# Performance work log

Measured on AMD Instinct MI355X. Metric: run time of the kernel, lower is better.

## Reference

```python
import jax, jax.numpy as jnp
import numpy as np

B, T, C, HS = 8, 4096, 1024, 64  # batch, seq, n_embd, head_size


def setup_inputs() -> dict:
    key = jax.random.key(0)
    kx, kk, kq, kv = jax.random.split(key, 4)
    x = jax.random.normal(kx, (B, T, C), dtype=jnp.float32)
    # bias-free linear weights, stored as [in, out] like flax kernels
    s = 1.0 / np.sqrt(C)
    Wk = jax.random.normal(kk, (C, HS), dtype=jnp.float32) * s
    Wq = jax.random.normal(kq, (C, HS), dtype=jnp.float32) * s
    Wv = jax.random.normal(kv, (C, HS), dtype=jnp.float32) * s
    return {"x": x, "Wk": Wk, "Wq": Wq, "Wv": Wv}


def reference(x, Wk, Wq, Wv):
    # x: [B, T, C]
    Tq = x.shape[1]
    Cdim = x.shape[2]
    k = jnp.einsum('btc,ch->bth', x, Wk)  # [B,T,HS]
    q = jnp.einsum('btc,ch->bth', x, Wq)
    v = jnp.einsum('btc,ch->bth', x, Wv)
    # NOTE: original scales by C**-0.5 (full embed dim), not head_size**-0.5
    scale = Cdim ** (-0.5)
    wei = jnp.einsum('bth,bsh->bts', q, k) * scale  # [B,T,T]
    causal = jnp.tril(jnp.ones((Tq, Tq), dtype=bool))
    wei = jnp.where(causal, wei, -jnp.inf)
    wei = jax.nn.softmax(wei, axis=-1)
    out = jnp.einsum('bts,bsh->bth', wei, v)  # [B,T,HS]
    return out
```

## Files before the change

kernel.cpp:

```cpp
#include <hip/hip_runtime.h>
#include <hip/hip_bf16.h>


typedef __attribute__((ext_vector_type(8))) short short8;
typedef __attribute__((ext_vector_type(4))) float f32x4;

#define NB 8
#define NT 4096
#define NC 1024
#define NH 64

__device__ __forceinline__ unsigned short f2bf(float f) {
    unsigned int u = __builtin_bit_cast(unsigned int, f);
    u += 0x7fffu + ((u >> 16) & 1u);
    return (unsigned short)(u >> 16);
}

__device__ __forceinline__ unsigned cvt_pk_bf16(float lo, float hi) {
    unsigned r;
    asm("v_cvt_pk_bf16_f32 %0, %1, %2" : "=v"(r) : "v"(lo), "v"(hi));
    return r;
}

#define GLOAD16(gp, lp)                                                        \
    __builtin_amdgcn_global_load_lds(                                          \
        (const __attribute__((address_space(1))) void*)(gp),                   \
        (__attribute__((address_space(3))) void*)(lp), 16, 0, 0)

__global__ __launch_bounds__(256) void wprep_kernel(
    const float* __restrict__ Wk, const float* __restrict__ Wq,
    const float* __restrict__ Wv, unsigned short* __restrict__ Wt)
{
    int n = blockIdx.x;
    int which = n >> 6, h = n & 63;
    const float* W = (which == 0) ? Wk : (which == 1) ? Wq : Wv;
    for (int c = threadIdx.x; c < NC; c += 256)
        Wt[(size_t)n * NC + c] = f2bf(W[(size_t)c * NH + h]);
}

__global__ __launch_bounds__(256, 2) void proj_kernel(
    const float* __restrict__ x, const unsigned short* __restrict__ Wt,
    unsigned short* __restrict__ qws, unsigned short* __restrict__ kws,
    unsigned short* __restrict__ vtws)
{
    __shared__ char lds[4][20480];

    const int lane = threadIdx.x & 63;
    const int wave = threadIdx.x >> 6;
    const int l15 = lane & 15;
    const int kg = lane >> 4;
    const int m0 = blockIdx.x * 64;

    const int agS = (lane & 7) ^ (lane >> 3);
    const float* aSrc[2];
#pragma unroll
    for (int j = 0; j < 2; ++j) {
        int i = wave * 2 + j;
        int r = 8 * i + (lane >> 3);
        aSrc[j] = x + (size_t)(m0 + r) * NC + agS * 4;
    }
    const int bgS = (lane & 3) ^ ((lane >> 2) & 3);
    const unsigned short* bSrc[3];
#pragma unroll
    for (int j = 0; j < 3; ++j) {
        int u = wave * 3 + j;
        int r = 16 * u + (lane >> 2);
        bSrc[j] = Wt + (size_t)r * NC + bgS * 8;
    }

    f32x4 acc[12];
#pragma unroll
    for (int i = 0; i < 12; ++i) acc[i] = f32x4{0.f, 0.f, 0.f, 0.f};

#define STAGE_CHUNK(c)                                                         \
    do {                                                                       \
        char* base_ = lds[(c) & 3];                                            \
        _Pragma("unroll")                                                      \
        for (int j = 0; j < 2; ++j)                                            \
            GLOAD16(aSrc[j] + (c) * 32, base_ + (wave * 2 + j) * 1024);        \
        _Pragma("unroll")                                                      \
        for (int j = 0; j < 3; ++j)                                            \
            GLOAD16(bSrc[j] + (c) * 32, base_ + 8192 + (wave * 3 + j) * 1024); \
    } while (0)

    STAGE_CHUNK(0);
    STAGE_CHUNK(1);

    for (int kc = 0; kc < 32; ++kc) {
        if (kc < 30) {
            STAGE_CHUNK(kc + 2);
            asm volatile("s_waitcnt vmcnt(10)" ::: "memory");
        } else if (kc == 30) {
            asm volatile("s_waitcnt vmcnt(5)" ::: "memory");
        } else {
            asm volatile("s_waitcnt vmcnt(0)" ::: "memory");
        }
        __builtin_amdgcn_sched_barrier(0);
        __builtin_amdgcn_s_barrier();

        const char* Ab = lds[kc & 3];
        const char* Bb = lds[kc & 3] + 8192;
        {
            const int r = wave * 16 + l15;
            const int g0 = kg * 2;
            f32x4 a0 = *(const f32x4*)(Ab + r * 128 + ((g0 ^ (r & 7)) * 16));
            f32x4 a1 = *(const f32x4*)(Ab + r * 128 + (((g0 + 1) ^ (r & 7)) * 16));
            short8 a;
            a[0] = (short)f2bf(a0[0]); a[1] = (short)f2bf(a0[1]);
            a[2] = (short)f2bf(a0[2]); a[3] = (short)f2bf(a0[3]);
            a[4] = (short)f2bf(a1[0]); a[5] = (short)f2bf(a1[1]);
            a[6] = (short)f2bf(a1[2]); a[7] = (short)f2bf(a1[3]);
#pragma unroll
            for (int nt = 0; nt < 12; ++nt) {
                int rb = nt * 16 + l15;
                short8 bfrag = *(const short8*)(
                    Bb + rb * 64 + ((kg ^ (rb & 3)) * 16));
                acc[nt] = __builtin_amdgcn_mfma_f32_16x16x32_bf16(a, bfrag, acc[nt], 0, 0, 0);
            }
        }
    }
#undef STAGE_CHUNK

    const float cs = 0.04508422f;
    const int crow0 = m0 + wave * 16 + (kg << 2);
#pragma unroll
    for (int nt = 0; nt < 12; ++nt) {
        int n = nt * 16 + l15;
        int which = n >> 6;
        int h = n & 63;
#pragma unroll
        for (int r = 0; r < 4; ++r) {
            int gm = crow0 + r;
            float av = acc[nt][r];
            if (which == 1) av *= cs;
            unsigned short v = f2bf(av);
            if (which == 0) {
                kws[(size_t)gm * NH + h] = v;
            } else if (which == 1) {
                qws[(size_t)gm * NH + h] = v;
            } else {
                int bb = gm >> 12, tt = gm & 4095;
                vtws[((size_t)(bb * NH + h)) * NT + tt] = v;
            }
        }
    }
}

__global__ __launch_bounds__(256) void flash_kernel(
    const unsigned short* __restrict__ qws, const unsigned short* __restrict__ kws,
    const unsigned short* __restrict__ vtws,
    float* __restrict__ opart, float* __restrict__ mlpart)
{
    __shared__ unsigned short Kbuf[2][64 * 64];
    __shared__ unsigned short Vbuf[2][64 * 64];
    __shared__ unsigned short Plds[4 * 16 * 64];

    const int id = blockIdx.x;
    const int kvh = id >> 9;
    const int rem9 = id & 511;
    const int lighthalf = rem9 >> 8;
    const int rem = rem9 & 255;
    const int b = rem & 7;
    const int i32 = rem >> 3;
    const int qt = lighthalf ? i32 : (63 - i32);
    const int nkv = qt + 1;
    const int hsp = nkv - (nkv >> 1);
    const int k0 = kvh ? hsp : 0;
    const int k1 = kvh ? nkv : hsp;
    const int pid_ = (kvh << 9) | ((b << 6) | qt);

    float* mlp = mlpart + (size_t)pid_ * 128;
    float* op  = opart + (size_t)pid_ * 4096;

    if (k0 >= k1) {
        f32x4 z = f32x4{0.f, 0.f, 0.f, 0.f};
        f32x4* op4 = (f32x4*)op;
        for (int i = threadIdx.x; i < 1024; i += 256) op4[i] = z;
        if (threadIdx.x < 64) {
            mlp[threadIdx.x] = -INFINITY;
            mlp[64 + threadIdx.x] = 0.f;
        }
        return;
    }

    const int lane = threadIdx.x & 63;
    const int wave = threadIdx.x >> 6;
    const int l15 = lane & 15;
    const int kg = lane >> 4;

    const int sg = (lane & 7) ^ (lane >> 3);
    const unsigned short* kSrc[2];
    const unsigned short* vSrc[2];
#pragma unroll
    for (int j = 0; j < 2; ++j) {
        int r = 16 * wave + 8 * j + (lane >> 3);
        kSrc[j] = kws + ((size_t)(b * NT) + r) * NH + sg * 8;
        vSrc[j] = vtws + ((size_t)(b * NH + r)) * NT + sg * 8;
    }

    short8 qf[2];
    {
        const unsigned short* qp =
            qws + ((size_t)(b * NT + qt * 64 + wave * 16 + l15)) * NH + kg * 8;
        qf[0] = *(const short8*)(qp);
        qf[1] = *(const short8*)(qp + 32);
    }

    f32x4 o[4];
#pragma unroll
    for (int dt = 0; dt < 4; ++dt) o[dt] = f32x4{0.f, 0.f, 0.f, 0.f};
    float m_r = -INFINITY;
    float l_r = 0.f;

    char* pw = (char*)Plds + wave * 2048;
    const int pswz = (l15 & 7) << 4;

#pragma unroll
    for (int j = 0; j < 2; ++j) {
        int i = 2 * wave + j;
        GLOAD16(kSrc[j] + (size_t)k0 * 64 * NH, (char*)Kbuf[0] + i * 1024);
        GLOAD16(vSrc[j] + (size_t)k0 * 64,      (char*)Vbuf[0] + i * 1024);
    }
    __syncthreads();

    int cur = 0;
    for (int kv = k0; kv < k1; ++kv) {
        if (kv + 1 < k1) {
#pragma unroll
            for (int j = 0; j < 2; ++j) {
                int i = 2 * wave + j;
                GLOAD16(kSrc[j] + (size_t)(kv + 1) * 64 * NH,
                        (char*)Kbuf[cur ^ 1] + i * 1024);
                GLOAD16(vSrc[j] + (size_t)(kv + 1) * 64,
                        (char*)Vbuf[cur ^ 1] + i * 1024);
            }
        }

        const char* Kb = (const char*)Kbuf[cur];
        const char* Vb = (const char*)Vbuf[cur];

        f32x4 st[4];
#pragma unroll
        for (int jt = 0; jt < 4; ++jt) st[jt] = f32x4{0.f, 0.f, 0.f, 0.f};
#pragma unroll
        for (int ks = 0; ks < 2; ++ks) {
            const int cbb = ks * 64 + kg * 16;
#pragma unroll
            for (int jt = 0; jt < 4; ++jt) {
                int krow = jt * 16 + l15;
                short8 kf = *(const short8*)(Kb + krow * 128 +
                                             (cbb ^ ((krow & 7) << 4)));
                st[jt] = __builtin_amdgcn_mfma_f32_16x16x32_bf16(kf, qf[ks], st[jt], 0, 0, 0);
            }
        }

        if (kv == qt) {
#pragma unroll
            for (int jt = 0; jt < 4; ++jt)
#pragma unroll
                for (int r = 0; r < 4; ++r)
                    if (jt * 16 + (kg << 2) + r > wave * 16 + l15)
                        st[jt][r] = -1e30f;
        }

        float lmax;
        {
            float t0 = fmaxf(fmaxf(st[0][0], st[0][1]), fmaxf(st[0][2], st[0][3]));
            float t1 = fmaxf(fmaxf(st[1][0], st[1][1]), fmaxf(st[1][2], st[1][3]));
            float t2 = fmaxf(fmaxf(st[2][0], st[2][1]), fmaxf(st[2][2], st[2][3]));
            float t3 = fmaxf(fmaxf(st[3][0], st[3][1]), fmaxf(st[3][2], st[3][3]));
            lmax = fmaxf(fmaxf(t0, t1), fmaxf(t2, t3));
        }

        if (!__all(lmax <= m_r + 8.0f)) {
            float pmax = lmax;
            pmax = fmaxf(pmax, __shfl_xor(pmax, 16));
            pmax = fmaxf(pmax, __shfl_xor(pmax, 32));
            float mn = fmaxf(m_r, pmax);
            float alpha = __builtin_amdgcn_exp2f(m_r - mn);
            m_r = mn;
            l_r *= alpha;
#pragma unroll
            for (int dt = 0; dt < 4; ++dt)
#pragma unroll
                for (int r = 0; r < 4; ++r)
                    o[dt][r] *= alpha;
        }

#pragma unroll
        for (int jt = 0; jt < 4; ++jt)
#pragma unroll
            for (int r = 0; r < 4; ++r)
                st[jt][r] = __builtin_amdgcn_exp2f(st[jt][r] - m_r);
        {
            float t0 = (st[0][0] + st[0][1]) + (st[0][2] + st[0][3]);
            float t1 = (st[1][0] + st[1][1]) + (st[1][2] + st[1][3]);
            float t2 = (st[2][0] + st[2][1]) + (st[2][2] + st[2][3]);
            float t3 = (st[3][0] + st[3][1]) + (st[3][2] + st[3][3]);
            l_r += (t0 + t1) + (t2 + t3);
        }

#pragma unroll
        for (int jt = 0; jt < 4; ++jt) {
            unsigned w0 = cvt_pk_bf16(st[jt][0], st[jt][1]);
            unsigned w1 = cvt_pk_bf16(st[jt][2], st[jt][3]);
            uint2 t; t.x = w0; t.y = w1;
            *(uint2*)(pw + l15 * 128 + ((jt * 32 + kg * 8) ^ pswz)) = t;
        }
        short8 pf[2];
#pragma unroll
        for (int ks = 0; ks < 2; ++ks)
            pf[ks] = *(const short8*)(pw + l15 * 128 + ((ks * 64 + kg * 16) ^ pswz));

#pragma unroll
        for (int ks = 0; ks < 2; ++ks) {
            const int cbb = ks * 64 + kg * 16;
#pragma unroll
            for (int dt = 0; dt < 4; ++dt) {
                int vrow = dt * 16 + l15;
                short8 vf = *(const short8*)(Vb + vrow * 128 +
                                             (cbb ^ ((vrow & 7) << 4)));
                o[dt] = __builtin_amdgcn_mfma_f32_16x16x32_bf16(vf, pf[ks], o[dt], 0, 0, 0);
            }
        }

        __syncthreads();
        cur ^= 1;
    }

    float lsum = l_r;
    lsum += __shfl_xor(lsum, 16);
    lsum += __shfl_xor(lsum, 32);
    float* orow = op + (wave * 16 + l15) * 64 + (kg << 2);
#pragma unroll
    for (int dt = 0; dt < 4; ++dt)
        *(f32x4*)(orow + dt * 16) = o[dt];
    if (kg == 0) {
        int q = wave * 16 + l15;
        mlp[q] = m_r;
        mlp[64 + q] = lsum;
    }
}

__global__ __launch_bounds__(256) void combine_kernel(
    const float* __restrict__ opart, const float* __restrict__ mlpart,
    float* __restrict__ out)
{
    const int cid = blockIdx.x;
    const int b = cid >> 6, qt = cid & 63;
    const float* mlA = mlpart + (size_t)cid * 128;
    const float* mlB = mlpart + (size_t)(512 + cid) * 128;
    const f32x4* oA = (const f32x4*)(opart + (size_t)cid * 4096);
    const f32x4* oB = (const f32x4*)(opart + (size_t)(512 + cid) * 4096);
    f32x4* og = (f32x4*)out;

#pragma unroll
    for (int i = 0; i < 4; ++i) {
        int g = threadIdx.x + i * 256;
        int row = g >> 4;
        float mA = mlA[row], lA = mlA[64 + row];
        float mB = mlB[row], lB = mlB[64 + row];
        float ms = fmaxf(mA, mB);
        float eA = __builtin_amdgcn_exp2f(mA - ms);
        float eB = __builtin_amdgcn_exp2f(mB - ms);
        float dinv = __builtin_amdgcn_rcpf(eA * lA + eB * lB);
        f32x4 a = oA[g], c = oB[g];
        f32x4 r;
        r[0] = (eA * a[0] + eB * c[0]) * dinv;
        r[1] = (eA * a[1] + eB * c[1]) * dinv;
        r[2] = (eA * a[2] + eB * c[2]) * dinv;
        r[3] = (eA * a[3] + eB * c[3]) * dinv;
        og[((size_t)(b * NT) + qt * 64 + row) * 16 + (g & 15)] = r;
    }
}

extern "C" void kernel_launch(void* const* d_in, const int* in_sizes, int n_in,
                              void* d_out, int out_size, void* d_ws, size_t ws_size,
                              hipStream_t stream) {
    const float* x  = (const float*)d_in[0];
    const float* Wk = (const float*)d_in[1];
    const float* Wq = (const float*)d_in[2];
    const float* Wv = (const float*)d_in[3];
    float* out = (float*)d_out;

    unsigned short* ws   = (unsigned short*)d_ws;
    const size_t qkv_elems = (size_t)NB * NT * NH;
    unsigned short* qws  = ws;
    unsigned short* kws  = qws + qkv_elems;
    unsigned short* vtws = kws + qkv_elems;
    unsigned short* Wt   = vtws + qkv_elems;
    float* opart  = (float*)(Wt + (size_t)192 * NC);
    float* mlpart = opart + (size_t)1024 * 4096;

    wprep_kernel<<<dim3(192), dim3(256), 0, stream>>>(Wk, Wq, Wv, Wt);
    proj_kernel<<<dim3(512), dim3(256), 0, stream>>>(x, Wt, qws, kws, vtws);
    flash_kernel<<<dim3(1024), dim3(256), 0, stream>>>(qws, kws, vtws, opart, mlpart);
    combine_kernel<<<dim3(512), dim3(256), 0, stream>>>(opart, mlpart, out);
}
```

Baseline: 86.96 us.

## Use 32x32 MFMA with 128-row query tiles and 4-way KV split

```diff
diff --git a/kernel.cpp b/kernel.cpp
--- a/kernel.cpp
+++ b/kernel.cpp
@@ -4,6 +4,8 @@
 
 typedef __attribute__((ext_vector_type(8))) short short8;
 typedef __attribute__((ext_vector_type(4))) float f32x4;
+typedef __attribute__((ext_vector_type(16))) float f32x16;
+typedef __attribute__((ext_vector_type(4))) unsigned int u32x4;
 
 #define NB 8
 #define NT 4096
@@ -146,47 +148,34 @@
     }
 }
 
-__global__ __launch_bounds__(256) void flash_kernel(
+__global__ __launch_bounds__(256, 4) void flash_kernel(
     const unsigned short* __restrict__ qws, const unsigned short* __restrict__ kws,
     const unsigned short* __restrict__ vtws,
     float* __restrict__ opart, float* __restrict__ mlpart)
 {
     __shared__ unsigned short Kbuf[2][64 * 64];
     __shared__ unsigned short Vbuf[2][64 * 64];
-    __shared__ unsigned short Plds[4 * 16 * 64];
 
     const int id = blockIdx.x;
-    const int kvh = id >> 9;
-    const int rem9 = id & 511;
-    const int lighthalf = rem9 >> 8;
-    const int rem = rem9 & 255;
-    const int b = rem & 7;
-    const int i32 = rem >> 3;
-    const int qt = lighthalf ? i32 : (63 - i32);
-    const int nkv = qt + 1;
-    const int hsp = nkv - (nkv >> 1);
-    const int k0 = kvh ? hsp : 0;
-    const int k1 = kvh ? nkv : hsp;
-    const int pid_ = (kvh << 9) | ((b << 6) | qt);
-
-    float* mlp = mlpart + (size_t)pid_ * 128;
-    float* op  = opart + (size_t)pid_ * 4096;
-
-    if (k0 >= k1) {
-        f32x4 z = f32x4{0.f, 0.f, 0.f, 0.f};
-        f32x4* op4 = (f32x4*)op;
-        for (int i = threadIdx.x; i < 1024; i += 256) op4[i] = z;
-        if (threadIdx.x < 64) {
-            mlp[threadIdx.x] = -INFINITY;
-            mlp[64 + threadIdx.x] = 0.f;
-        }
-        return;
-    }
+    const int g = id >> 5;
+    const int p = (id >> 3) & 3;
+    const int b = id & 7;
+    const int a = g & 7, m = g >> 3;
+    const int qt = (m == 0) ? 31 - a : (m == 1) ? 16 + a : (m == 2) ? 15 - a : a;
+    const int n = 2 * qt + 2;
+    const int len = (n + 3) >> 2;
+    const int k0 = p * len;
+    const int k1 = (k0 + len < n) ? (k0 + len) : n;
+    const int pid = id;
+
+    float* mlp = mlpart + (size_t)pid * 256;
+    float* op  = opart + (size_t)pid * 8192;
 
     const int lane = threadIdx.x & 63;
     const int wave = threadIdx.x >> 6;
-    const int l15 = lane & 15;
-    const int kg = lane >> 4;
+    const int l31 = lane & 31;
+    const int hi = lane >> 5;
+    const int rsw = lane & 7;
 
     const int sg = (lane & 7) ^ (lane >> 3);
     const unsigned short* kSrc[2];
@@ -198,28 +187,27 @@
         vSrc[j] = vtws + ((size_t)(b * NH + r)) * NT + sg * 8;
     }
 
-    short8 qf[2];
+    const int qmin = qt * 128 + wave * 32;
+    short8 qf[4];
     {
-        const unsigned short* qp =
-            qws + ((size_t)(b * NT + qt * 64 + wave * 16 + l15)) * NH + kg * 8;
-        qf[0] = *(const short8*)(qp);
-        qf[1] = *(const short8*)(qp + 32);
-    }
-
-    f32x4 o[4];
-#pragma unroll
-    for (int dt = 0; dt < 4; ++dt) o[dt] = f32x4{0.f, 0.f, 0.f, 0.f};
+        const char* qp = (const char*)(qws + ((size_t)(b * NT) + qmin + l31) * NH);
+#pragma unroll
+        for (int s = 0; s < 4; ++s)
+            qf[s] = *(const short8*)(qp + s * 32 + hi * 16);
+    }
+
+    f32x16 o0, o1;
+#pragma unroll
+    for (int i = 0; i < 16; ++i) { o0[i] = 0.f; o1[i] = 0.f; }
     float m_r = -INFINITY;
     float l_r = 0.f;
 
-    char* pw = (char*)Plds + wave * 2048;
-    const int pswz = (l15 & 7) << 4;
-
+    const int kst = (k0 < n) ? k0 : (n - 1);
 #pragma unroll
     for (int j = 0; j < 2; ++j) {
         int i = 2 * wave + j;
-        GLOAD16(kSrc[j] + (size_t)k0 * 64 * NH, (char*)Kbuf[0] + i * 1024);
-        GLOAD16(vSrc[j] + (size_t)k0 * 64,      (char*)Vbuf[0] + i * 1024);
+        GLOAD16(kSrc[j] + (size_t)kst * 64 * NH, (char*)Kbuf[0] + i * 1024);
+        GLOAD16(vSrc[j] + (size_t)kst * 64,      (char*)Vbuf[0] + i * 1024);
     }
     __syncthreads();
 
@@ -239,106 +227,105 @@
         const char* Kb = (const char*)Kbuf[cur];
         const char* Vb = (const char*)Vbuf[cur];
 
-        f32x4 st[4];
-#pragma unroll
-        for (int jt = 0; jt < 4; ++jt) st[jt] = f32x4{0.f, 0.f, 0.f, 0.f};
-#pragma unroll
-        for (int ks = 0; ks < 2; ++ks) {
-            const int cbb = ks * 64 + kg * 16;
-#pragma unroll
-            for (int jt = 0; jt < 4; ++jt) {
-                int krow = jt * 16 + l15;
-                short8 kf = *(const short8*)(Kb + krow * 128 +
-                                             (cbb ^ ((krow & 7) << 4)));
-                st[jt] = __builtin_amdgcn_mfma_f32_16x16x32_bf16(kf, qf[ks], st[jt], 0, 0, 0);
-            }
-        }
-
-        if (kv == qt) {
-#pragma unroll
-            for (int jt = 0; jt < 4; ++jt)
-#pragma unroll
-                for (int r = 0; r < 4; ++r)
-                    if (jt * 16 + (kg << 2) + r > wave * 16 + l15)
-                        st[jt][r] = -1e30f;
-        }
-
-        float lmax;
-        {
-            float t0 = fmaxf(fmaxf(st[0][0], st[0][1]), fmaxf(st[0][2], st[0][3]));
-            float t1 = fmaxf(fmaxf(st[1][0], st[1][1]), fmaxf(st[1][2], st[1][3]));
-            float t2 = fmaxf(fmaxf(st[2][0], st[2][1]), fmaxf(st[2][2], st[2][3]));
-            float t3 = fmaxf(fmaxf(st[3][0], st[3][1]), fmaxf(st[3][2], st[3][3]));
-            lmax = fmaxf(fmaxf(t0, t1), fmaxf(t2, t3));
-        }
+        f32x16 st0, st1;
+#pragma unroll
+        for (int i = 0; i < 16; ++i) { st0[i] = 0.f; st1[i] = 0.f; }
+        __builtin_amdgcn_s_setprio(1);
+#pragma unroll
+        for (int s = 0; s < 4; ++s) {
+            int gl = s * 2 + hi;
+            short8 ka = *(const short8*)(Kb + l31 * 128 + ((gl ^ rsw) << 4));
+            short8 kb = *(const short8*)(Kb + (32 + l31) * 128 + ((gl ^ rsw) << 4));
+            st0 = __builtin_amdgcn_mfma_f32_32x32x16_bf16(ka, qf[s], st0, 0, 0, 0);
+            st1 = __builtin_amdgcn_mfma_f32_32x32x16_bf16(kb, qf[s], st1, 0, 0, 0);
+        }
+        __builtin_amdgcn_s_setprio(0);
+
+        const int kb0 = kv * 64;
+        if (kb0 + 63 > qmin) {
+            const int qg = qmin + l31;
+#pragma unroll
+            for (int r = 0; r < 16; ++r) {
+                int key = kb0 + (r & 3) + 8 * (r >> 2) + 4 * hi;
+                if (key > qg) st0[r] = -1e30f;
+                if (key + 32 > qg) st1[r] = -1e30f;
+            }
+        }
+
+        float lmax = st0[0];
+#pragma unroll
+        for (int r = 1; r < 16; ++r) lmax = fmaxf(lmax, st0[r]);
+#pragma unroll
+        for (int r = 0; r < 16; ++r) lmax = fmaxf(lmax, st1[r]);
 
         if (!__all(lmax <= m_r + 8.0f)) {
-            float pmax = lmax;
-            pmax = fmaxf(pmax, __shfl_xor(pmax, 16));
-            pmax = fmaxf(pmax, __shfl_xor(pmax, 32));
+            float pmax = fmaxf(lmax, __shfl_xor(lmax, 32));
             float mn = fmaxf(m_r, pmax);
             float alpha = __builtin_amdgcn_exp2f(m_r - mn);
             m_r = mn;
             l_r *= alpha;
 #pragma unroll
-            for (int dt = 0; dt < 4; ++dt)
-#pragma unroll
-                for (int r = 0; r < 4; ++r)
-                    o[dt][r] *= alpha;
-        }
-
-#pragma unroll
-        for (int jt = 0; jt < 4; ++jt)
-#pragma unroll
-            for (int r = 0; r < 4; ++r)
-                st[jt][r] = __builtin_amdgcn_exp2f(st[jt][r] - m_r);
-        {
-            float t0 = (st[0][0] + st[0][1]) + (st[0][2] + st[0][3]);
-            float t1 = (st[1][0] + st[1][1]) + (st[1][2] + st[1][3]);
-            float t2 = (st[2][0] + st[2][1]) + (st[2][2] + st[2][3]);
-            float t3 = (st[3][0] + st[3][1]) + (st[3][2] + st[3][3]);
-            l_r += (t0 + t1) + (t2 + t3);
-        }
-
-#pragma unroll
-        for (int jt = 0; jt < 4; ++jt) {
-            unsigned w0 = cvt_pk_bf16(st[jt][0], st[jt][1]);
-            unsigned w1 = cvt_pk_bf16(st[jt][2], st[jt][3]);
-            uint2 t; t.x = w0; t.y = w1;
-            *(uint2*)(pw + l15 * 128 + ((jt * 32 + kg * 8) ^ pswz)) = t;
-        }
-        short8 pf[2];
-#pragma unroll
-        for (int ks = 0; ks < 2; ++ks)
-            pf[ks] = *(const short8*)(pw + l15 * 128 + ((ks * 64 + kg * 16) ^ pswz));
-
-#pragma unroll
-        for (int ks = 0; ks < 2; ++ks) {
-            const int cbb = ks * 64 + kg * 16;
-#pragma unroll
-            for (int dt = 0; dt < 4; ++dt) {
-                int vrow = dt * 16 + l15;
-                short8 vf = *(const short8*)(Vb + vrow * 128 +
-                                             (cbb ^ ((vrow & 7) << 4)));
-                o[dt] = __builtin_amdgcn_mfma_f32_16x16x32_bf16(vf, pf[ks], o[dt], 0, 0, 0);
-            }
-        }
+            for (int r = 0; r < 16; ++r) { o0[r] *= alpha; o1[r] *= alpha; }
+        }
+
+        float psum = 0.f;
+#pragma unroll
+        for (int r = 0; r < 16; ++r) {
+            st0[r] = __builtin_amdgcn_exp2f(st0[r] - m_r);
+            st1[r] = __builtin_amdgcn_exp2f(st1[r] - m_r);
+            psum += st0[r] + st1[r];
+        }
+        l_r += psum;
+
+        __builtin_amdgcn_s_setprio(1);
+#pragma unroll
+        for (int kt = 0; kt < 2; ++kt) {
+            const f32x16& st = kt ? st1 : st0;
+            unsigned pa0 = cvt_pk_bf16(st[0], st[1]),  pa1 = cvt_pk_bf16(st[2], st[3]);
+            unsigned pb0 = cvt_pk_bf16(st[4], st[5]),  pb1 = cvt_pk_bf16(st[6], st[7]);
+            unsigned pc0 = cvt_pk_bf16(st[8], st[9]),  pc1 = cvt_pk_bf16(st[10], st[11]);
+            unsigned pd0 = cvt_pk_bf16(st[12], st[13]), pd1 = cvt_pk_bf16(st[14], st[15]);
+            unsigned xa0 = __shfl_xor((int)pa0, 32), xa1 = __shfl_xor((int)pa1, 32);
+            unsigned xb0 = __shfl_xor((int)pb0, 32), xb1 = __shfl_xor((int)pb1, 32);
+            unsigned xc0 = __shfl_xor((int)pc0, 32), xc1 = __shfl_xor((int)pc1, 32);
+            unsigned xd0 = __shfl_xor((int)pd0, 32), xd1 = __shfl_xor((int)pd1, 32);
+            u32x4 wA, wB;
+            wA[0] = hi ? xb0 : pa0;  wA[1] = hi ? xb1 : pa1;
+            wA[2] = hi ? pb0 : xa0;  wA[3] = hi ? pb1 : xa1;
+            wB[0] = hi ? xd0 : pc0;  wB[1] = hi ? xd1 : pc1;
+            wB[2] = hi ? pd0 : xc0;  wB[3] = hi ? pd1 : xc1;
+            short8 pfA = __builtin_bit_cast(short8, wA);
+            short8 pfB = __builtin_bit_cast(short8, wB);
+#pragma unroll
+            for (int w = 0; w < 2; ++w) {
+                short8 pf = w ? pfB : pfA;
+                int gv = (kt * 2 + w) * 2 + hi;
+                short8 va = *(const short8*)(Vb + l31 * 128 + ((gv ^ rsw) << 4));
+                short8 vb = *(const short8*)(Vb + (32 + l31) * 128 + ((gv ^ rsw) << 4));
+                o0 = __builtin_amdgcn_mfma_f32_32x32x16_bf16(va, pf, o0, 0, 0, 0);
+                o1 = __builtin_amdgcn_mfma_f32_32x32x16_bf16(vb, pf, o1, 0, 0, 0);
+            }
+        }
+        __builtin_amdgcn_s_setprio(0);
 
         __syncthreads();
         cur ^= 1;
     }
 
-    float lsum = l_r;
-    lsum += __shfl_xor(lsum, 16);
-    lsum += __shfl_xor(lsum, 32);
-    float* orow = op + (wave * 16 + l15) * 64 + (kg << 2);
-#pragma unroll
-    for (int dt = 0; dt < 4; ++dt)
-        *(f32x4*)(orow + dt * 16) = o[dt];
-    if (kg == 0) {
-        int q = wave * 16 + l15;
-        mlp[q] = m_r;
-        mlp[64 + q] = lsum;
+    float lt = l_r + __shfl_xor(l_r, 32);
+    const int row = wave * 32 + l31;
+    float* orow = op + row * 64;
+#pragma unroll
+    for (int blk = 0; blk < 4; ++blk) {
+        f32x4 v0, v1;
+#pragma unroll
+        for (int r = 0; r < 4; ++r) { v0[r] = o0[blk * 4 + r]; v1[r] = o1[blk * 4 + r]; }
+        *(f32x4*)(orow + 8 * blk + 4 * hi) = v0;
+        *(f32x4*)(orow + 32 + 8 * blk + 4 * hi) = v1;
+    }
+    if (hi == 0) {
+        mlp[row] = m_r;
+        mlp[128 + row] = lt;
     }
 }
 
@@ -347,30 +334,42 @@
     float* __restrict__ out)
 {
     const int cid = blockIdx.x;
-    const int b = cid >> 6, qt = cid & 63;
-    const float* mlA = mlpart + (size_t)cid * 128;
-    const float* mlB = mlpart + (size_t)(512 + cid) * 128;
-    const f32x4* oA = (const f32x4*)(opart + (size_t)cid * 4096);
-    const f32x4* oB = (const f32x4*)(opart + (size_t)(512 + cid) * 4096);
+    const int qt = cid >> 3, b = cid & 7;
+    int g;
+    if (qt >= 24) g = 31 - qt;
+    else if (qt >= 16) g = 8 + (qt - 16);
+    else if (qt >= 8) g = 16 + (15 - qt);
+    else g = 24 + qt;
+    const int pidb = g * 32 + b;
+
+    const float* ml[4];
+    const f32x4* ov[4];
+#pragma unroll
+    for (int p = 0; p < 4; ++p) {
+        ml[p] = mlpart + (size_t)(pidb + p * 8) * 256;
+        ov[p] = (const f32x4*)(opart + (size_t)(pidb + p * 8) * 8192);
+    }
     f32x4* og = (f32x4*)out;
 
 #pragma unroll
-    for (int i = 0; i < 4; ++i) {
-        int g = threadIdx.x + i * 256;
-        int row = g >> 4;
-        float mA = mlA[row], lA = mlA[64 + row];
-        float mB = mlB[row], lB = mlB[64 + row];
-        float ms = fmaxf(mA, mB);
-        float eA = __builtin_amdgcn_exp2f(mA - ms);
-        float eB = __builtin_amdgcn_exp2f(mB - ms);
-        float dinv = __builtin_amdgcn_rcpf(eA * lA + eB * lB);
-        f32x4 a = oA[g], c = oB[g];
+    for (int i = 0; i < 8; ++i) {
+        int gidx = threadIdx.x + i * 256;
+        int row = gidx >> 4;
+        float m0 = ml[0][row], m1 = ml[1][row], m2 = ml[2][row], m3 = ml[3][row];
+        float ms = fmaxf(fmaxf(m0, m1), fmaxf(m2, m3));
+        float e0 = __builtin_amdgcn_exp2f(m0 - ms);
+        float e1 = __builtin_amdgcn_exp2f(m1 - ms);
+        float e2 = __builtin_amdgcn_exp2f(m2 - ms);
+        float e3 = __builtin_amdgcn_exp2f(m3 - ms);
+        float den = e0 * ml[0][128 + row] + e1 * ml[1][128 + row] +
+                    e2 * ml[2][128 + row] + e3 * ml[3][128 + row];
+        float dinv = __builtin_amdgcn_rcpf(den);
+        f32x4 a0 = ov[0][gidx], a1 = ov[1][gidx], a2 = ov[2][gidx], a3 = ov[3][gidx];
         f32x4 r;
-        r[0] = (eA * a[0] + eB * c[0]) * dinv;
-        r[1] = (eA * a[1] + eB * c[1]) * dinv;
-        r[2] = (eA * a[2] + eB * c[2]) * dinv;
-        r[3] = (eA * a[3] + eB * c[3]) * dinv;
-        og[((size_t)(b * NT) + qt * 64 + row) * 16 + (g & 15)] = r;
+#pragma unroll
+        for (int c = 0; c < 4; ++c)
+            r[c] = (e0 * a0[c] + e1 * a1[c] + e2 * a2[c] + e3 * a3[c]) * dinv;
+        og[((size_t)(b * NT) + qt * 128 + row) * 16 + (gidx & 15)] = r;
     }
 }
 
@@ -390,10 +389,10 @@
     unsigned short* vtws = kws + qkv_elems;
     unsigned short* Wt   = vtws + qkv_elems;
     float* opart  = (float*)(Wt + (size_t)192 * NC);
-    float* mlpart = opart + (size_t)1024 * 4096;
+    float* mlpart = opart + (size_t)1024 * 8192;
 
     wprep_kernel<<<dim3(192), dim3(256), 0, stream>>>(Wk, Wq, Wv, Wt);
     proj_kernel<<<dim3(512), dim3(256), 0, stream>>>(x, Wt, qws, kws, vtws);
     flash_kernel<<<dim3(1024), dim3(256), 0, stream>>>(qws, kws, vtws, opart, mlpart);
-    combine_kernel<<<dim3(512), dim3(256), 0, stream>>>(opart, mlpart, out);
-}
+    combine_kernel<<<dim3(256), dim3(256), 0, stream>>>(opart, mlpart, out);
+}
```

Result: faster. 79.53 us (-8.5%).
